# Optimization experiments

Hardware: AMD Instinct MI355X
Metric: run time of the kernel (lower is better)

## Reference

```python
import jax, jax.numpy as jnp
import numpy as np

EMBED = 768; HEADS = 12; MLP = 3072
WL_IN = 4        # activation bits (signed)
WL_W = 4         # weight bits (bit-sliced into 1-bit RRAM cells)
ADC = 5          # ADC precision for each analog partial sum
SUBARRAY = 128   # crossbar subArray rows
ONOFF = 10.0     # conductance on/off ratio
VARI = 0.02      # conductance variability
EPS = 1e-5


def _adc_quant(y, bits):
    # Linear ADC quantization over the full observed range.
    ymax = jnp.max(jnp.abs(y))
    step = ymax / (2 ** bits - 1)
    step = jnp.where(step > 0, step, jnp.ones_like(step))
    return jnp.round(y / step) * step


def _qlinear(x, W, b, key):
    # RRAM crossbar simulated linear layer. x: [T, Fin], W: [Fout, Fin].
    upper, lower = 1.0, 1.0 / ONOFF
    T, Fin = x.shape
    Fout = W.shape[0]
    Wlev = 2 ** WL_W - 1
    Xlev = 2 ** (WL_IN - 1) - 1
    # --- weight -> unsigned integer levels -> binary cell conductances ---
    wmax = jnp.max(jnp.abs(W))
    Wdec = jnp.round((W / wmax + 1.0) * 0.5 * Wlev).astype(jnp.int32)   # [Fout,Fin] in [0,Wlev]
    kb = jnp.arange(WL_W)
    wbits = ((Wdec[:, :, None] >> kb) & 1).astype(x.dtype)              # [Fout,Fin,K]
    noise = VARI * jax.random.normal(key, wbits.shape, dtype=x.dtype)   # conductance variability
    cond = (wbits * (upper - lower) + lower) * (1.0 + noise)
    dummy = 0.5 * (upper + lower)                                       # dummy column conductance
    # --- activation -> signed integer -> magnitude bit slices ---
    xmax = jnp.max(jnp.abs(x))
    Xq = jnp.round(x / xmax * Xlev).astype(jnp.int32)
    sgn = jnp.sign(Xq).astype(x.dtype)
    zb = jnp.arange(WL_IN - 1)
    xbits = ((jnp.abs(Xq)[:, :, None] >> zb) & 1).astype(x.dtype) * sgn[:, :, None]  # [T,Fin,Z]
    # --- subArray partitioning along input dim ---
    pad = (-Fin) % SUBARRAY
    if pad:
        xbits = jnp.pad(xbits, ((0, 0), (0, pad), (0, 0)))
        cond = jnp.pad(cond, ((0, 0), (0, pad), (0, 0)))
    nc = (Fin + pad) // SUBARRAY
    xb = xbits.reshape(T, nc, SUBARRAY, WL_IN - 1)
    cb = cond.reshape(Fout, nc, SUBARRAY, WL_W)
    # analog MAC per subarray, per (input bit z, weight cell k)
    partial = jnp.einsum('tcsz,ocsk->tcozk', xb, cb)                    # [T,nc,Fout,Z,K]
    dummyP = dummy * xb.sum(axis=2)                                     # [T,nc,Z]
    partialQ = _adc_quant(partial, ADC)
    dummyQ = _adc_quant(dummyP, ADC)
    net = partialQ - dummyQ[:, :, None, :, None]                        # recenter to signed weights
    scale = (2.0 ** zb)[:, None] * (2.0 ** kb)[None, :]                 # [Z,K] shift-add
    acc = jnp.einsum('tcozk,zk->to', net, scale)
    out = acc * (xmax / Xlev) * (2.0 * wmax / ((upper - lower) * Wlev))
    return out + b


def _layernorm(x, g, b):
    mu = jnp.mean(x, axis=-1, keepdims=True)
    var = jnp.var(x, axis=-1, keepdims=True)
    return (x - mu) * jax.lax.rsqrt(var + EPS) * g + b


def _attention(x, in_w, in_b, out_w, out_b):
    L, N, E = x.shape
    D = E // HEADS
    qkv = x @ in_w.T + in_b                                             # [L,N,3E]
    q, k, v = jnp.split(qkv, 3, axis=-1)
    q = q.reshape(L, N, HEADS, D)
    k = k.reshape(L, N, HEADS, D)
    v = v.reshape(L, N, HEADS, D)
    scores = jnp.einsum('lnhd,mnhd->nhlm', q, k) / jnp.sqrt(jnp.asarray(D, x.dtype))
    attn = jax.nn.softmax(scores, axis=-1)
    ctx = jnp.einsum('nhlm,mnhd->lnhd', attn, v).reshape(L, N, E)
    return ctx @ out_w.T + out_b


def setup_inputs() -> dict:
    key = jax.random.key(0)
    ks = jax.random.split(key, 8)
    s = 0.02
    return {
        'x': jax.random.normal(ks[0], (256, 2, EMBED), jnp.float32),
        'in_proj_w': s * jax.random.normal(ks[1], (3 * EMBED, EMBED), jnp.float32),
        'in_proj_b': jnp.zeros((3 * EMBED,), jnp.float32),
        'out_proj_w': s * jax.random.normal(ks[2], (EMBED, EMBED), jnp.float32),
        'out_proj_b': jnp.zeros((EMBED,), jnp.float32),
        'ln1_g': jnp.ones((EMBED,), jnp.float32),
        'ln1_b': jnp.zeros((EMBED,), jnp.float32),
        'W1': s * jax.random.normal(ks[3], (MLP, EMBED), jnp.float32),
        'b1': jnp.zeros((MLP,), jnp.float32),
        'W2': s * jax.random.normal(ks[4], (EMBED, MLP), jnp.float32),
        'b2': jnp.zeros((EMBED,), jnp.float32),
        'ln2_g': jnp.ones((EMBED,), jnp.float32),
        'ln2_b': jnp.zeros((EMBED,), jnp.float32),
    }


def reference(x, in_proj_w, in_proj_b, out_proj_w, out_proj_b,
              ln1_g, ln1_b, W1, b1, W2, b2, ln2_g, ln2_b):
    L, N, E = x.shape
    a = _attention(x, in_proj_w, in_proj_b, out_proj_w, out_proj_b)
    h = _layernorm(x + a, ln1_g, ln1_b)
    t = h.reshape(L * N, E)
    m = _qlinear(t, W1, b1, jax.random.key(1))
    m = jax.nn.gelu(m, approximate=False)   # torch nn.GELU default = exact erf
    m = _qlinear(m, W2, b2, jax.random.key(2))
    m = m.reshape(L, N, E)
    return _layernorm(h + m, ln2_g, ln2_b)
```

## Files before the change

### kernel.cpp

```cpp
#include <hip/hip_runtime.h>
#include <math.h>
#include <stdint.h>

#define TOK   512
#define EMB   768
#define QKVD  2304
#define NHEAD 12
#define HD    64
#define MLPD  3072
#define SUBA  128

#define OFF_QKV      0ull
#define OFF_SCORES   9437184ull
#define OFF_CTX      22020096ull
#define OFF_H1PRE    25165824ull
#define OFF_H1       26738688ull
#define OFF_M1       28311552ull
#define OFF_X2       34603008ull
#define OFF_M2       40894464ull
#define OFF_DQ1      42467328ull
#define OFF_DQ2      42504192ull
#define OFF_SCAL     42651648ull
#define OFF_NOISE1   42651712ull
#define OFF_NOISE2   80400448ull
#define OFF_SUMXB1   118149184ull
#define OFF_SUMXB2   118186048ull
#define OFF_WDEC1    118333504ull
#define OFF_WDEC2    120692800ull
#define OFF_XQT1     123052096ull
#define OFF_XQT2     123445312ull
#define WS_NEEDED    125018176ull


__device__ __forceinline__ void blockMaxAtomic(double v, unsigned long long* slot, double* red){
  int tid = threadIdx.x;
  red[tid] = v; __syncthreads();
  for (int st = 128; st > 0; st >>= 1){
    if (tid < st){ double o = red[tid+st]; if (o > red[tid]) red[tid] = o; }
    __syncthreads();
  }
  if (tid == 0) atomicMax(slot, (unsigned long long)__double_as_longlong(red[0]));
}

__device__ __forceinline__ double readSlot(const unsigned long long* s){
  return __longlong_as_double((long long)(*s));
}

__device__ __forceinline__ float xla_exp_f32(float _x){
  float x = fminf(_x, 88.3762626647950f);
  x = fmaxf(x, -88.3762626647949f);
  float m = floorf(fmaf(x, 1.44269504088896341f, 0.5f));
  float r = fmaf(m, -0.6931471805599453f, x);
  float r2 = __fmul_rn(r, r);
  float r3 = __fmul_rn(r2, r);
  float y  = fmaf(1.9875691500e-4f, r, 1.3981999507e-3f);
  float y1 = fmaf(4.1665795894e-2f, r, 1.6666665459e-1f);
  float y2 = __fadd_rn(r, 1.0f);
  y  = fmaf(y, r, 8.3334519073e-3f);
  y1 = fmaf(y1, r, 5.0000001201e-1f);
  y  = fmaf(y, r3, y1);
  y  = fmaf(y, r2, y2);
  int mi = (int)m;
  float two_m = __uint_as_float((unsigned)((mi + 127) << 23));
  float res = __fmul_rn(y, two_m);
  return fmaxf(res, _x);
}

__device__ __forceinline__ float xla_erf_f32(float v){
  float x = fmaxf(fminf(v, 4.0f), -4.0f);
  float x2 = __fmul_rn(x, x);
  float p = fmaf(x2, -2.72614225801306e-10f, 2.77068142495902e-08f);
  p = fmaf(x2, p, -2.10102402082508e-06f);
  p = fmaf(x2, p, -5.69250639462346e-05f);
  p = fmaf(x2, p, -7.34990630326855e-04f);
  p = fmaf(x2, p, -2.95459980854025e-03f);
  p = fmaf(x2, p, -1.60960333262415e-02f);
  p = __fmul_rn(x, p);
  float q = fmaf(x2, -1.45660718464996e-05f, -2.13374055278905e-04f);
  q = fmaf(x2, q, -1.68282697438203e-03f);
  q = fmaf(x2, q, -7.37332916720468e-03f);
  q = fmaf(x2, q, -1.42647390514189e-02f);
  return __fdiv_rn(p, q);
}

__device__ __forceinline__ uint32_t rotl32(uint32_t x, int r){ return (x << r) | (x >> (32 - r)); }

__device__ __forceinline__ void threefry2x32(uint32_t k0, uint32_t k1,
                                             uint32_t x0, uint32_t x1,
                                             uint32_t& o0, uint32_t& o1){
  uint32_t ks2 = k0 ^ k1 ^ 0x1BD11BDAu;
  x0 += k0; x1 += k1;
#define TF_R(r) { x0 += x1; x1 = rotl32(x1, r); x1 ^= x0; }
  TF_R(13) TF_R(15) TF_R(26) TF_R(6)
  x0 += k1; x1 += ks2 + 1u;
  TF_R(17) TF_R(29) TF_R(16) TF_R(24)
  x0 += ks2; x1 += k0 + 2u;
  TF_R(13) TF_R(15) TF_R(26) TF_R(6)
  x0 += k0; x1 += k1 + 3u;
  TF_R(17) TF_R(29) TF_R(16) TF_R(24)
  x0 += k1; x1 += ks2 + 4u;
  TF_R(13) TF_R(15) TF_R(26) TF_R(6)
  x0 += ks2; x1 += k0 + 5u;
#undef TF_R
  o0 = x0; o1 = x1;
}

__device__ float bits_to_noise(uint32_t bits){
  uint32_t fb = (bits >> 9) | 0x3f800000u;
  float f = __uint_as_float(fb);
  f = __fadd_rn(f, -1.0f);
  const float lo = -0.99999994f;
  float u = __fadd_rn(__fmul_rn(f, 2.0f), lo);
  u = fmaxf(lo, u);
  float x  = u;
  float xx = __fmul_rn(x, x);
  float nx = -xx;
  float l1p;
  if (fabsf(nx) < 1e-4f){
    l1p = __fmul_rn(__fadd_rn(__fmul_rn(-0.5f, nx), 1.0f), nx);
  } else {
    float u1 = __fadd_rn(nx, 1.0f);
    l1p = (float)log((double)u1);
  }
  float w = -l1p;
  float p;
  if (w < 5.0f){
    w = __fadd_rn(w, -2.5f);
    p = 2.81022636e-08f;
    p = __fadd_rn(3.43273939e-07f, __fmul_rn(p, w));
    p = __fadd_rn(-3.5233877e-06f,  __fmul_rn(p, w));
    p = __fadd_rn(-4.39150654e-06f, __fmul_rn(p, w));
    p = __fadd_rn(0.00021858087f,   __fmul_rn(p, w));
    p = __fadd_rn(-0.00125372503f,  __fmul_rn(p, w));
    p = __fadd_rn(-0.00417768164f,  __fmul_rn(p, w));
    p = __fadd_rn(0.246640727f,     __fmul_rn(p, w));
    p = __fadd_rn(1.50140941f,      __fmul_rn(p, w));
  } else {
    float sw = __fsqrt_rn(w);
    w = __fadd_rn(sw, -3.0f);
    p = -0.000200214257f;
    p = __fadd_rn(0.000100950558f, __fmul_rn(p, w));
    p = __fadd_rn(0.00134934322f,  __fmul_rn(p, w));
    p = __fadd_rn(-0.00367342844f, __fmul_rn(p, w));
    p = __fadd_rn(0.00573950773f,  __fmul_rn(p, w));
    p = __fadd_rn(-0.0076224613f,  __fmul_rn(p, w));
    p = __fadd_rn(0.00943887047f,  __fmul_rn(p, w));
    p = __fadd_rn(1.00167406f,     __fmul_rn(p, w));
    p = __fadd_rn(2.83297682f,     __fmul_rn(p, w));
  }
  float ei  = __fmul_rn(p, x);
  float nrm = __fmul_rn(1.41421354f, ei);
  return __fmul_rn(0.02f, nrm);
}

__global__ void absmax_f32_k(const float* p, int n, unsigned long long* slot){
  __shared__ double red[256];
  double m = 0.0;
  for (int i = blockIdx.x*256 + threadIdx.x; i < n; i += gridDim.x*256){
    double v = fabs((double)p[i]); if (v > m) m = v;
  }
  blockMaxAtomic(m, slot, red);
}

__global__ void noise_gen_k(uint32_t k0, uint32_t k1, unsigned int n, float* noise){
  unsigned int i = blockIdx.x*256u + threadIdx.x;
  if (i >= n) return;
  uint32_t o0, o1;
  threefry2x32(k0, k1, 0u, i, o0, o1);
  noise[i] = bits_to_noise(o0 ^ o1);
}

__global__ void wdec_gen_k(const float* W, int nW, const unsigned long long* wmax_slot,
                           unsigned char* Wdec){
  int i = blockIdx.x*256 + threadIdx.x;
  if (i >= nW) return;
  float wmax = (float)readSlot(wmax_slot);
  float d = __fdiv_rn(W[i], wmax);
  d = __fadd_rn(d, 1.0f);
  d = __fmul_rn(d, 0.5f);
  d = __fmul_rn(d, 15.0f);
  Wdec[i] = (unsigned char)(int)rintf(d);
}

__global__ __launch_bounds__(256) void qkv_gemm_k(const float* x, const float* w, const float* b, float* qkv){
  __shared__ float xt[8][EMB];
  int j  = blockIdx.x*256 + threadIdx.x;
  int t0 = blockIdx.y*8;
  for (int v = threadIdx.x; v < 8*EMB; v += 256){
    int tt = v / EMB, e = v % EMB;
    xt[tt][e] = x[(size_t)(t0+tt)*EMB + e];
  }
  __syncthreads();
  float acc[8] = {0,0,0,0,0,0,0,0};
  const float* wr = w + (size_t)j*EMB;
  for (int e = 0; e < EMB; ++e){
    float wv = wr[e];
#pragma unroll
    for (int tt = 0; tt < 8; ++tt) acc[tt] = fmaf(xt[tt][e], wv, acc[tt]);
  }
  float bv = b[j];
  for (int tt = 0; tt < 8; ++tt)
    qkv[(size_t)(t0+tt)*QKVD + j] = __fadd_rn(acc[tt], bv);
}

__global__ __launch_bounds__(256) void attn_scores_k(const float* qkv, float* sc){
  __shared__ float kt[32][HD+1];
  int nh = blockIdx.x;
  int n  = nh / NHEAD, h = nh % NHEAD;
  int m0 = blockIdx.y * 32;
  int l  = threadIdx.x;
  for (int v = threadIdx.x; v < 32*HD; v += 256){
    int mm = v / HD, d = v % HD;
    kt[mm][d] = qkv[(size_t)((m0+mm)*2 + n)*QKVD + EMB + h*HD + d];
  }
  __syncthreads();
  float acc[32];
#pragma unroll
  for (int mm = 0; mm < 32; ++mm) acc[mm] = 0.0f;
  const float* qrow = qkv + (size_t)(l*2 + n)*QKVD + h*HD;
  for (int d = 0; d < HD; ++d){
    float qv = qrow[d];
#pragma unroll
    for (int mm = 0; mm < 32; ++mm) acc[mm] = fmaf(qv, kt[mm][d], acc[mm]);
  }
  float* srow = sc + ((size_t)nh*256 + l)*256 + m0;
#pragma unroll
  for (int mm = 0; mm < 32; ++mm) srow[mm] = __fdiv_rn(acc[mm], 8.0f);
}

__global__ void softmax_rows_k(float* sc){
  int row = blockIdx.x*256 + threadIdx.x;
  if (row >= 24*256) return;
  float* p = sc + (size_t)row*256;
  float mx = p[0];
  for (int m = 1; m < 256; ++m) mx = fmaxf(mx, p[m]);
  for (int m = 0; m < 256; ++m) p[m] = xla_exp_f32(__fsub_rn(p[m], mx));
  float s = 0.0f;
  for (int m = 0; m < 256; ++m) s = __fadd_rn(s, p[m]);
  for (int m = 0; m < 256; ++m) p[m] = __fdiv_rn(p[m], s);
}

__global__ void attn_ctx_k(const float* sc, const float* qkv, float* ctx){
  int idx = blockIdx.x*256 + threadIdx.x;
  int t = idx / EMB, i = idx % EMB;
  int l = t / 2, n = t % 2, h = i / HD;
  const float* arow = sc + ((size_t)(n*NHEAD + h)*256 + l)*256;
  float acc = 0.0f;
  for (int m = 0; m < 256; ++m)
    acc = fmaf(arow[m], qkv[(size_t)(m*2 + n)*QKVD + 1536 + i], acc);
  ctx[(size_t)t*EMB + i] = acc;
}

__global__ __launch_bounds__(256) void outproj_res_k(const float* ctx, const float* w, const float* b,
                                                     const float* x, float* h1pre){
  __shared__ float ct[8][EMB];
  int e  = blockIdx.x*256 + threadIdx.x;
  int t0 = blockIdx.y*8;
  for (int v = threadIdx.x; v < 8*EMB; v += 256){
    int tt = v / EMB, i = v % EMB;
    ct[tt][i] = ctx[(size_t)(t0+tt)*EMB + i];
  }
  __syncthreads();
  float acc[8] = {0,0,0,0,0,0,0,0};
  const float* wr = w + (size_t)e*EMB;
  for (int i = 0; i < EMB; ++i){
    float wv = wr[i];
#pragma unroll
    for (int tt = 0; tt < 8; ++tt) acc[tt] = fmaf(ct[tt][i], wv, acc[tt]);
  }
  float bv = b[e];
  for (int tt = 0; tt < 8; ++tt){
    size_t t = t0 + tt;
    float af = __fadd_rn(acc[tt], bv);
    h1pre[t*EMB + e] = __fadd_rn(x[t*EMB + e], af);
  }
}

__global__ void ln_rows_k(const float* in, const float* g, const float* b, float* out){
  int t = blockIdx.x*256 + threadIdx.x;
  if (t >= TOK) return;
  const float* p = in + (size_t)t*EMB;
  float s = 0.0f;
  for (int e = 0; e < EMB; ++e) s = __fadd_rn(s, p[e]);
  float mu = __fdiv_rn(s, 768.0f);
  float s2 = 0.0f;
  for (int e = 0; e < EMB; ++e){
    float d = __fsub_rn(p[e], mu);
    s2 = __fadd_rn(s2, __fmul_rn(d, d));
  }
  float var = __fdiv_rn(s2, 768.0f);
  float rs = __fdiv_rn(1.0f, __fsqrt_rn(__fadd_rn(var, 1e-5f)));
  for (int e = 0; e < EMB; ++e){
    float d = __fsub_rn(p[e], mu);
    out[(size_t)t*EMB + e] = __fadd_rn(__fmul_rn(__fmul_rn(d, rs), g[e]), b[e]);
  }
}

__global__ void final_ln_rows_k(const float* h1, const float* m2T, const float* g, const float* b, float* out){
  int t = blockIdx.x*256 + threadIdx.x;
  if (t >= TOK) return;
  const float* p = h1 + (size_t)t*EMB;
  float s = 0.0f;
  for (int e = 0; e < EMB; ++e) s = __fadd_rn(s, __fadd_rn(p[e], m2T[(size_t)e*TOK + t]));
  float mu = __fdiv_rn(s, 768.0f);
  float s2 = 0.0f;
  for (int e = 0; e < EMB; ++e){
    float d = __fsub_rn(__fadd_rn(p[e], m2T[(size_t)e*TOK + t]), mu);
    s2 = __fadd_rn(s2, __fmul_rn(d, d));
  }
  float var = __fdiv_rn(s2, 768.0f);
  float rs = __fdiv_rn(1.0f, __fsqrt_rn(__fadd_rn(var, 1e-5f)));
  for (int e = 0; e < EMB; ++e){
    float d = __fsub_rn(__fadd_rn(p[e], m2T[(size_t)e*TOK + t]), mu);
    out[(size_t)t*EMB + e] = __fadd_rn(__fmul_rn(__fmul_rn(d, rs), g[e]), b[e]);
  }
}

__global__ void quantx_k(const float* val, const unsigned long long* xmax_slot, int Fin,
                         signed char* XqT){
  int idx = blockIdx.x*256 + threadIdx.x;
  if (idx >= TOK*Fin) return;
  int t = idx / Fin, i = idx % Fin;
  float xmax = (float)readSlot(xmax_slot);
  float u = __fmul_rn(__fdiv_rn(val[idx], xmax), 7.0f);
  XqT[(size_t)i*TOK + t] = (signed char)(int)rintf(u);
}

__global__ void quantxT_k(const float* valT, const unsigned long long* xmax_slot, int n,
                          signed char* XqT){
  int idx = blockIdx.x*256 + threadIdx.x;
  if (idx >= n) return;
  float xmax = (float)readSlot(xmax_slot);
  float u = __fmul_rn(__fdiv_rn(valT[idx], xmax), 7.0f);
  XqT[idx] = (signed char)(int)rintf(u);
}

__global__ void sumxb_k(const signed char* XqT, int NC, int* sumxb, unsigned long long* dmax_slot){
  int idx = blockIdx.x*256 + threadIdx.x;
  if (idx >= TOK*NC) return;
  int t = idx / NC, c = idx % NC;
  int n0 = 0, n1 = 0, n2 = 0;
  for (int s = 0; s < SUBA; ++s){
    int q = XqT[(size_t)(c*SUBA + s)*TOK + t];
    int a = q < 0 ? -q : q;
    int sg = (q > 0) - (q < 0);
    n0 += (a & 1) * sg; n1 += ((a >> 1) & 1) * sg; n2 += ((a >> 2) & 1) * sg;
  }
  sumxb[idx*3 + 0] = n0; sumxb[idx*3 + 1] = n1; sumxb[idx*3 + 2] = n2;
  float d0 = fabsf(__fmul_rn(0.55f, (float)n0));
  float d1 = fabsf(__fmul_rn(0.55f, (float)n1));
  float d2 = fabsf(__fmul_rn(0.55f, (float)n2));
  float m = fmaxf(d0, fmaxf(d1, d2));
  atomicMax(dmax_slot, (unsigned long long)__double_as_longlong((double)m));
}

__global__ void dummyq_k(const int* sumxb, int NC, const unsigned long long* dmax_slot, float* dqT){
  int idx = blockIdx.x*256 + threadIdx.x;
  if (idx >= TOK*NC*3) return;
  int t = idx / (NC*3);
  int r = idx % (NC*3);
  int c = r / 3, z = r % 3;
  float dmax = (float)readSlot(dmax_slot);
  float step = __fdiv_rn(dmax, 31.0f);
  if (!(step > 0.0f)) step = 1.0f;
  float P = __fmul_rn(0.55f, (float)sumxb[idx]);
  dqT[((size_t)c*3 + z)*TOK + t] = __fmul_rn(rintf(__fdiv_rn(P, step)), step);
}

template<int OTILE>
__device__ __forceinline__ void qlin_stage(const signed char* XqT, const unsigned char* Wdec,
                                           const float* noise, int Fin, int c, int o0, int t0,
                                           signed char* xq, float (*cond)[SUBA][4]){
  const int tid = threadIdx.x;
  const uint32_t* src = (const uint32_t*)(XqT + (size_t)c*SUBA*TOK + t0);
  uint32_t* dst = (uint32_t*)xq;
  for (int j = tid; j < SUBA*64; j += 256){
    int s = j >> 6, dw = j & 63;
    dst[s*64 + dw] = src[s*128 + dw];
  }
  for (int v = tid; v < OTILE*SUBA*4; v += 256){
    int o = v >> 9;
    int r = v & 511;
    int s = r >> 2, k = r & 3;
    size_t i = (size_t)(o0+o)*Fin + c*SUBA + s;
    float bit = (float)((Wdec[i] >> k) & 1);
    float nz  = noise[i*4 + k];
    cond[o][s][k] = __fmul_rn(__fadd_rn(__fmul_rn(bit, 0.9f), 0.1f), __fadd_rn(1.0f, nz));
  }
}

template<int OTILE>
__device__ __forceinline__ void qlin_acc_c(const signed char* xq, const float (*cond)[SUBA][4],
                                           float (*acc)[12]){
  const int tid = threadIdx.x;
#pragma unroll
  for (int o = 0; o < OTILE; ++o)
#pragma unroll
    for (int r = 0; r < 12; ++r) acc[o][r] = 0.0f;
  for (int s = 0; s < SUBA; ++s){
    int q = xq[s*256 + tid];
    int a = q < 0 ? -q : q;
    int i0 = a & 1, i1 = (a >> 1) & 1, i2 = (a >> 2) & 1;
    if (q < 0){ i0 = -i0; i1 = -i1; i2 = -i2; }
    float b0 = (float)i0, b1 = (float)i1, b2 = (float)i2;
#pragma unroll
    for (int o = 0; o < OTILE; ++o){
      const float4 cv = *(const float4*)&cond[o][s][0];
      acc[o][0]  = fmaf(b0, cv.x, acc[o][0]);
      acc[o][1]  = fmaf(b0, cv.y, acc[o][1]);
      acc[o][2]  = fmaf(b0, cv.z, acc[o][2]);
      acc[o][3]  = fmaf(b0, cv.w, acc[o][3]);
      acc[o][4]  = fmaf(b1, cv.x, acc[o][4]);
      acc[o][5]  = fmaf(b1, cv.y, acc[o][5]);
      acc[o][6]  = fmaf(b1, cv.z, acc[o][6]);
      acc[o][7]  = fmaf(b1, cv.w, acc[o][7]);
      acc[o][8]  = fmaf(b2, cv.x, acc[o][8]);
      acc[o][9]  = fmaf(b2, cv.y, acc[o][9]);
      acc[o][10] = fmaf(b2, cv.z, acc[o][10]);
      acc[o][11] = fmaf(b2, cv.w, acc[o][11]);
    }
  }
}

template<int OTILE>
__global__ __launch_bounds__(256) void qlin_pass1_t(const signed char* XqT, const unsigned char* Wdec,
                                                    const float* noise, int Fin, int NC,
                                                    unsigned long long* ymax_slot){
  __shared__ signed char xq[SUBA*256];
  __shared__ float cond[OTILE][SUBA][4];
  __shared__ double red[256];
  const int o0 = blockIdx.x*OTILE;
  const int t0 = blockIdx.y*256;
  float acc[OTILE][12];
  float lmax = 0.0f;
  for (int c = 0; c < NC; ++c){
    __syncthreads();
    qlin_stage<OTILE>(XqT, Wdec, noise, Fin, c, o0, t0, xq, cond);
    __syncthreads();
    qlin_acc_c<OTILE>(xq, cond, acc);
#pragma unroll
    for (int o = 0; o < OTILE; ++o)
#pragma unroll
      for (int r = 0; r < 12; ++r) lmax = fmaxf(lmax, fabsf(acc[o][r]));
  }
  blockMaxAtomic((double)lmax, ymax_slot, red);
}

template<int OTILE>
__global__ __launch_bounds__(256) void qlin_pass2_t(const signed char* XqT, const unsigned char* Wdec,
                                                    const float* noise, const float* dqT, const float* bias,
                                                    int Fin, int NC,
                                                    const unsigned long long* ymax_slot,
                                                    const unsigned long long* xmax_slot,
                                                    const unsigned long long* wmax_slot,
                                                    float* outT){
  __shared__ signed char xq[SUBA*256];
  __shared__ float cond[OTILE][SUBA][4];
  const int o0 = blockIdx.x*OTILE;
  const int t0 = blockIdx.y*256;
  const int t  = t0 + threadIdx.x;
  float ymax = (float)readSlot(ymax_slot);
  float step = __fdiv_rn(ymax, 31.0f);
  if (!(step > 0.0f)) step = 1.0f;
  float acc[OTILE][12];
  float netsum[OTILE][12];
#pragma unroll
  for (int o = 0; o < OTILE; ++o)
#pragma unroll
    for (int r = 0; r < 12; ++r) netsum[o][r] = 0.0f;
  for (int c = 0; c < NC; ++c){
    __syncthreads();
    qlin_stage<OTILE>(XqT, Wdec, noise, Fin, c, o0, t0, xq, cond);
    __syncthreads();
    qlin_acc_c<OTILE>(xq, cond, acc);
    float dqv[3];
#pragma unroll
    for (int z = 0; z < 3; ++z) dqv[z] = dqT[((size_t)c*3 + z)*TOK + t];
#pragma unroll
    for (int o = 0; o < OTILE; ++o)
#pragma unroll
      for (int z = 0; z < 3; ++z)
#pragma unroll
        for (int k = 0; k < 4; ++k){
          float pq  = __fmul_rn(rintf(__fdiv_rn(acc[o][z*4+k], step)), step);
          float net = __fsub_rn(pq, dqv[z]);
          netsum[o][z*4+k] = __fadd_rn(netsum[o][z*4+k], net);
        }
  }
  float xmax = (float)readSlot(xmax_slot);
  float wmax = (float)readSlot(wmax_slot);
  float A = __fdiv_rn(xmax, 7.0f);
  float B = __fdiv_rn(__fmul_rn(2.0f, wmax), 13.5f);
#pragma unroll
  for (int o = 0; o < OTILE; ++o){
    float tot = 0.0f;
#pragma unroll
    for (int z = 0; z < 3; ++z)
#pragma unroll
      for (int k = 0; k < 4; ++k)
        tot = __fadd_rn(tot, __fmul_rn(netsum[o][z*4+k], (float)(1 << (z + k))));
    float outv = __fadd_rn(__fmul_rn(__fmul_rn(tot, A), B), bias[o0+o]);
    outT[(size_t)(o0+o)*TOK + t] = outv;
  }
}

__global__ void gelu_absmax_k(const float* m1, int n, float* x2, unsigned long long* xmax_slot){
  __shared__ double red[256];
  double m = 0.0;
  for (int i = blockIdx.x*256 + threadIdx.x; i < n; i += gridDim.x*256){
    float v = m1[i];
    float t1 = __fdiv_rn(v, 1.4142135623730951f);
    float e = xla_erf_f32(t1);
    float s = __fadd_rn(e, 1.0f);
    float g = __fdiv_rn(__fmul_rn(v, s), 2.0f);
    x2[i] = g;
    double a = fabs((double)g); if (a > m) m = a;
  }
  blockMaxAtomic(m, xmax_slot, red);
}

extern "C" void kernel_launch(void* const* d_in, const int* in_sizes, int n_in,
                              void* d_out, int out_size, void* d_ws, size_t ws_size,
                              hipStream_t stream){
  if (ws_size < WS_NEEDED) return;
  const float* x      = (const float*)d_in[0];
  const float* in_w   = (const float*)d_in[1];
  const float* in_b   = (const float*)d_in[2];
  const float* out_w  = (const float*)d_in[3];
  const float* out_b  = (const float*)d_in[4];
  const float* ln1_g  = (const float*)d_in[5];
  const float* ln1_b  = (const float*)d_in[6];
  const float* W1     = (const float*)d_in[7];
  const float* b1     = (const float*)d_in[8];
  const float* W2     = (const float*)d_in[9];
  const float* b2     = (const float*)d_in[10];
  const float* ln2_g  = (const float*)d_in[11];
  const float* ln2_b  = (const float*)d_in[12];

  char* ws = (char*)d_ws;
  float* qkv    = (float*)(ws + OFF_QKV);
  float* scores = (float*)(ws + OFF_SCORES);
  float* ctx    = (float*)(ws + OFF_CTX);
  float* h1pre  = (float*)(ws + OFF_H1PRE);
  float* h1     = (float*)(ws + OFF_H1);
  float* m1     = (float*)(ws + OFF_M1);
  float* x2     = (float*)(ws + OFF_X2);
  float* m2     = (float*)(ws + OFF_M2);
  float* dq1    = (float*)(ws + OFF_DQ1);
  float* dq2    = (float*)(ws + OFF_DQ2);
  unsigned long long* scal = (unsigned long long*)(ws + OFF_SCAL);
  float* noise1  = (float*)(ws + OFF_NOISE1);
  float* noise2  = (float*)(ws + OFF_NOISE2);
  int*   sumxb1  = (int*)(ws + OFF_SUMXB1);
  int*   sumxb2  = (int*)(ws + OFF_SUMXB2);
  unsigned char* wdec1 = (unsigned char*)(ws + OFF_WDEC1);
  unsigned char* wdec2 = (unsigned char*)(ws + OFF_WDEC2);
  signed char* xqt1 = (signed char*)(ws + OFF_XQT1);
  signed char* xqt2 = (signed char*)(ws + OFF_XQT2);

  hipMemsetAsync(scal, 0, 64, stream);

  absmax_f32_k<<<1024,256,0,stream>>>(W1, MLPD*EMB, scal+0);
  absmax_f32_k<<<1024,256,0,stream>>>(W2, EMB*MLPD, scal+1);

  noise_gen_k<<<36864,256,0,stream>>>(0u, 1u, 9437184u, noise1);
  noise_gen_k<<<36864,256,0,stream>>>(0u, 2u, 9437184u, noise2);
  wdec_gen_k<<<9216,256,0,stream>>>(W1, MLPD*EMB, scal+0, wdec1);
  wdec_gen_k<<<9216,256,0,stream>>>(W2, EMB*MLPD, scal+1, wdec2);

  qkv_gemm_k<<<dim3(9,64),256,0,stream>>>(x, in_w, in_b, qkv);
  attn_scores_k<<<dim3(24,8),256,0,stream>>>(qkv, scores);
  softmax_rows_k<<<24,256,0,stream>>>(scores);
  attn_ctx_k<<<1536,256,0,stream>>>(scores, qkv, ctx);
  outproj_res_k<<<dim3(3,64),256,0,stream>>>(ctx, out_w, out_b, x, h1pre);
  ln_rows_k<<<2,256,0,stream>>>(h1pre, ln1_g, ln1_b, h1);

  absmax_f32_k<<<1024,256,0,stream>>>(h1, TOK*EMB, scal+2);
  quantx_k<<<(TOK*EMB+255)/256,256,0,stream>>>(h1, scal+2, EMB, xqt1);
  sumxb_k<<<(TOK*6+255)/256,256,0,stream>>>(xqt1, 6, sumxb1, scal+4);
  dummyq_k<<<(TOK*6*3+255)/256,256,0,stream>>>(sumxb1, 6, scal+4, dq1);
  qlin_pass1_t<8><<<dim3(MLPD/8,2),256,0,stream>>>(xqt1, wdec1, noise1, EMB, 6, scal+3);
  qlin_pass2_t<4><<<dim3(MLPD/4,2),256,0,stream>>>(xqt1, wdec1, noise1, dq1, b1,
                                                   EMB, 6, scal+3, scal+2, scal+0, m1);

  gelu_absmax_k<<<6144,256,0,stream>>>(m1, TOK*MLPD, x2, scal+5);
  quantxT_k<<<(TOK*MLPD+255)/256,256,0,stream>>>(x2, scal+5, TOK*MLPD, xqt2);
  sumxb_k<<<(TOK*24+255)/256,256,0,stream>>>(xqt2, 24, sumxb2, scal+7);
  dummyq_k<<<(TOK*24*3+255)/256,256,0,stream>>>(sumxb2, 24, scal+7, dq2);
  qlin_pass1_t<4><<<dim3(EMB/4,2),256,0,stream>>>(xqt2, wdec2, noise2, MLPD, 24, scal+6);
  qlin_pass2_t<4><<<dim3(EMB/4,2),256,0,stream>>>(xqt2, wdec2, noise2, dq2, b2,
                                                  MLPD, 24, scal+6, scal+5, scal+1, m2);

  final_ln_rows_k<<<2,256,0,stream>>>(h1, m2, ln2_g, ln2_b, (float*)d_out);
}
```

Measured before the change: 3.157 ms.

## Use packed FP32 FMA, tile GEMM weights in LDS, split pass1 over chunks

Replaces the scalar FMAs in the dense GEMMs, attention scores, attention context and the crossbar accumulation with two-wide packed FMA vectors (v_pk_fma_f32 on CDNA). The QKV and out-projection GEMMs are merged into one kernel that stages 32-wide K tiles of the weights in padded LDS rather than reading weight rows straight from global memory. The K tile in attention scores is transposed so that vector loads from it are contiguous, and attn_ctx now computes two outputs per thread. The ADC max pass1 kernels gain a z grid dimension that splits subarray chunks across blocks, which adds parallelism at the cost of more atomicMax operations.

```diff
diff --git a/kernel.cpp b/kernel.cpp
--- a/kernel.cpp
+++ b/kernel.cpp
@@ -31,6 +31,16 @@
 #define OFF_XQT2     123445312ull
 #define WS_NEEDED    125018176ull
 
+
+typedef float f32x2 __attribute__((ext_vector_type(2)));
+
+__device__ __forceinline__ f32x2 pkfma(f32x2 a, f32x2 b, f32x2 c){
+#if __has_builtin(__builtin_elementwise_fma)
+  return __builtin_elementwise_fma(a, b, c);
+#else
+  f32x2 r; r.x = fmaf(a.x, b.x, c.x); r.y = fmaf(a.y, b.y, c.y); return r;
+#endif
+}
 
 __device__ __forceinline__ void blockMaxAtomic(double v, unsigned long long* slot, double* red){
   int tid = threadIdx.x;
@@ -182,50 +192,79 @@
   Wdec[i] = (unsigned char)(int)rintf(d);
 }
 
-__global__ __launch_bounds__(256) void qkv_gemm_k(const float* x, const float* w, const float* b, float* qkv){
-  __shared__ float xt[8][EMB];
-  int j  = blockIdx.x*256 + threadIdx.x;
-  int t0 = blockIdx.y*8;
-  for (int v = threadIdx.x; v < 8*EMB; v += 256){
-    int tt = v / EMB, e = v % EMB;
-    xt[tt][e] = x[(size_t)(t0+tt)*EMB + e];
-  }
-  __syncthreads();
-  float acc[8] = {0,0,0,0,0,0,0,0};
-  const float* wr = w + (size_t)j*EMB;
-  for (int e = 0; e < EMB; ++e){
-    float wv = wr[e];
-#pragma unroll
-    for (int tt = 0; tt < 8; ++tt) acc[tt] = fmaf(xt[tt][e], wv, acc[tt]);
-  }
-  float bv = b[j];
-  for (int tt = 0; tt < 8; ++tt)
-    qkv[(size_t)(t0+tt)*QKVD + j] = __fadd_rn(acc[tt], bv);
+#define KTILE 32
+__global__ __launch_bounds__(256) void gemm8_k(const float* src, const float* w, const float* bias,
+                                               const float* resid, float* out, int N, int K){
+  __shared__ float xt[EMB*8];
+  __shared__ float wl[256*(KTILE+1)];
+  const int tid = threadIdx.x;
+  const int j  = blockIdx.x*256 + tid;
+  const int t0 = blockIdx.y*8;
+  for (int v = tid; v < K*8; v += 256){
+    int e = v >> 3, tt = v & 7;
+    xt[v] = src[(size_t)(t0+tt)*K + e];
+  }
+  f32x2 acc[4] = {{0.f,0.f},{0.f,0.f},{0.f,0.f},{0.f,0.f}};
+  const int ntile = K / KTILE;
+  for (int et = 0; et < ntile; ++et){
+    __syncthreads();
+    for (int v = tid; v < 256*KTILE; v += 256){
+      int r = v >> 5, cc = v & 31;
+      wl[r*(KTILE+1) + cc] = w[(size_t)(blockIdx.x*256 + r)*K + et*KTILE + cc];
+    }
+    __syncthreads();
+    for (int ee = 0; ee < KTILE; ++ee){
+      float wv = wl[tid*(KTILE+1) + ee];
+      f32x2 wv2 = {wv, wv};
+      const f32x2* xp = (const f32x2*)&xt[(et*KTILE + ee)*8];
+#pragma unroll
+      for (int q = 0; q < 4; ++q) acc[q] = pkfma(xp[q], wv2, acc[q]);
+    }
+  }
+  float bv = bias[j];
+#pragma unroll
+  for (int q = 0; q < 4; ++q){
+    float a0 = __fadd_rn(acc[q].x, bv);
+    float a1 = __fadd_rn(acc[q].y, bv);
+    size_t ta = (size_t)(t0 + q*2), tb = ta + 1;
+    if (resid){
+      out[ta*N + j] = __fadd_rn(resid[ta*N + j], a0);
+      out[tb*N + j] = __fadd_rn(resid[tb*N + j], a1);
+    } else {
+      out[ta*N + j] = a0;
+      out[tb*N + j] = a1;
+    }
+  }
 }
 
 __global__ __launch_bounds__(256) void attn_scores_k(const float* qkv, float* sc){
-  __shared__ float kt[32][HD+1];
+  __shared__ float kt[64][34];
   int nh = blockIdx.x;
   int n  = nh / NHEAD, h = nh % NHEAD;
   int m0 = blockIdx.y * 32;
   int l  = threadIdx.x;
-  for (int v = threadIdx.x; v < 32*HD; v += 256){
-    int mm = v / HD, d = v % HD;
-    kt[mm][d] = qkv[(size_t)((m0+mm)*2 + n)*QKVD + EMB + h*HD + d];
+  for (int v = threadIdx.x; v < 32*64; v += 256){
+    int mm = v >> 6, d = v & 63;
+    kt[d][mm] = qkv[(size_t)((m0+mm)*2 + n)*QKVD + EMB + h*HD + d];
   }
   __syncthreads();
-  float acc[32];
-#pragma unroll
-  for (int mm = 0; mm < 32; ++mm) acc[mm] = 0.0f;
+  f32x2 acc[16];
+#pragma unroll
+  for (int i = 0; i < 16; ++i) acc[i] = {0.f,0.f};
   const float* qrow = qkv + (size_t)(l*2 + n)*QKVD + h*HD;
   for (int d = 0; d < HD; ++d){
     float qv = qrow[d];
-#pragma unroll
-    for (int mm = 0; mm < 32; ++mm) acc[mm] = fmaf(qv, kt[mm][d], acc[mm]);
+    f32x2 q2 = {qv, qv};
+    const f32x2* kp = (const f32x2*)&kt[d][0];
+#pragma unroll
+    for (int i = 0; i < 16; ++i) acc[i] = pkfma(q2, kp[i], acc[i]);
   }
   float* srow = sc + ((size_t)nh*256 + l)*256 + m0;
 #pragma unroll
-  for (int mm = 0; mm < 32; ++mm) srow[mm] = __fdiv_rn(acc[mm], 8.0f);
+  for (int i = 0; i < 16; ++i){
+    srow[2*i]   = __fdiv_rn(acc[i].x, 8.0f);
+    srow[2*i+1] = __fdiv_rn(acc[i].y, 8.0f);
+  }
 }
 
 __global__ void softmax_rows_k(float* sc){
@@ -242,38 +281,19 @@
 
 __global__ void attn_ctx_k(const float* sc, const float* qkv, float* ctx){
   int idx = blockIdx.x*256 + threadIdx.x;
-  int t = idx / EMB, i = idx % EMB;
-  int l = t / 2, n = t % 2, h = i / HD;
+  int t = idx / 384, i2 = idx % 384;
+  int i = i2*2;
+  int l = t >> 1, n = t & 1, h = i >> 6;
   const float* arow = sc + ((size_t)(n*NHEAD + h)*256 + l)*256;
-  float acc = 0.0f;
-  for (int m = 0; m < 256; ++m)
-    acc = fmaf(arow[m], qkv[(size_t)(m*2 + n)*QKVD + 1536 + i], acc);
-  ctx[(size_t)t*EMB + i] = acc;
-}
-
-__global__ __launch_bounds__(256) void outproj_res_k(const float* ctx, const float* w, const float* b,
-                                                     const float* x, float* h1pre){
-  __shared__ float ct[8][EMB];
-  int e  = blockIdx.x*256 + threadIdx.x;
-  int t0 = blockIdx.y*8;
-  for (int v = threadIdx.x; v < 8*EMB; v += 256){
-    int tt = v / EMB, i = v % EMB;
-    ct[tt][i] = ctx[(size_t)(t0+tt)*EMB + i];
-  }
-  __syncthreads();
-  float acc[8] = {0,0,0,0,0,0,0,0};
-  const float* wr = w + (size_t)e*EMB;
-  for (int i = 0; i < EMB; ++i){
-    float wv = wr[i];
-#pragma unroll
-    for (int tt = 0; tt < 8; ++tt) acc[tt] = fmaf(ct[tt][i], wv, acc[tt]);
-  }
-  float bv = b[e];
-  for (int tt = 0; tt < 8; ++tt){
-    size_t t = t0 + tt;
-    float af = __fadd_rn(acc[tt], bv);
-    h1pre[t*EMB + e] = __fadd_rn(x[t*EMB + e], af);
-  }
+  f32x2 acc = {0.f,0.f};
+  for (int m = 0; m < 256; ++m){
+    float av = arow[m];
+    f32x2 a2 = {av, av};
+    f32x2 v2 = *(const f32x2*)&qkv[(size_t)(m*2 + n)*QKVD + 1536 + i];
+    acc = pkfma(a2, v2, acc);
+  }
+  ctx[(size_t)t*EMB + i]     = acc.x;
+  ctx[(size_t)t*EMB + i + 1] = acc.y;
 }
 
 __global__ void ln_rows_k(const float* in, const float* g, const float* b, float* out){
@@ -391,49 +411,46 @@
 
 template<int OTILE>
 __device__ __forceinline__ void qlin_acc_c(const signed char* xq, const float (*cond)[SUBA][4],
-                                           float (*acc)[12]){
+                                           f32x2 (*acc)[6]){
   const int tid = threadIdx.x;
 #pragma unroll
   for (int o = 0; o < OTILE; ++o)
 #pragma unroll
-    for (int r = 0; r < 12; ++r) acc[o][r] = 0.0f;
+    for (int r = 0; r < 6; ++r) acc[o][r] = {0.f,0.f};
   for (int s = 0; s < SUBA; ++s){
     int q = xq[s*256 + tid];
     int a = q < 0 ? -q : q;
     int i0 = a & 1, i1 = (a >> 1) & 1, i2 = (a >> 2) & 1;
     if (q < 0){ i0 = -i0; i1 = -i1; i2 = -i2; }
-    float b0 = (float)i0, b1 = (float)i1, b2 = (float)i2;
+    float f0 = (float)i0, f1 = (float)i1, f2 = (float)i2;
+    f32x2 b0 = {f0, f0}, b1 = {f1, f1}, b2 = {f2, f2};
 #pragma unroll
     for (int o = 0; o < OTILE; ++o){
-      const float4 cv = *(const float4*)&cond[o][s][0];
-      acc[o][0]  = fmaf(b0, cv.x, acc[o][0]);
-      acc[o][1]  = fmaf(b0, cv.y, acc[o][1]);
-      acc[o][2]  = fmaf(b0, cv.z, acc[o][2]);
-      acc[o][3]  = fmaf(b0, cv.w, acc[o][3]);
-      acc[o][4]  = fmaf(b1, cv.x, acc[o][4]);
-      acc[o][5]  = fmaf(b1, cv.y, acc[o][5]);
-      acc[o][6]  = fmaf(b1, cv.z, acc[o][6]);
-      acc[o][7]  = fmaf(b1, cv.w, acc[o][7]);
-      acc[o][8]  = fmaf(b2, cv.x, acc[o][8]);
-      acc[o][9]  = fmaf(b2, cv.y, acc[o][9]);
-      acc[o][10] = fmaf(b2, cv.z, acc[o][10]);
-      acc[o][11] = fmaf(b2, cv.w, acc[o][11]);
+      const f32x2* cp = (const f32x2*)&cond[o][s][0];
+      f32x2 c01 = cp[0], c23 = cp[1];
+      acc[o][0] = pkfma(b0, c01, acc[o][0]);
+      acc[o][1] = pkfma(b0, c23, acc[o][1]);
+      acc[o][2] = pkfma(b1, c01, acc[o][2]);
+      acc[o][3] = pkfma(b1, c23, acc[o][3]);
+      acc[o][4] = pkfma(b2, c01, acc[o][4]);
+      acc[o][5] = pkfma(b2, c23, acc[o][5]);
     }
   }
 }
 
-template<int OTILE>
+template<int OTILE, int CCHUNK>
 __global__ __launch_bounds__(256) void qlin_pass1_t(const signed char* XqT, const unsigned char* Wdec,
-                                                    const float* noise, int Fin, int NC,
+                                                    const float* noise, int Fin,
                                                     unsigned long long* ymax_slot){
   __shared__ signed char xq[SUBA*256];
   __shared__ float cond[OTILE][SUBA][4];
   __shared__ double red[256];
   const int o0 = blockIdx.x*OTILE;
   const int t0 = blockIdx.y*256;
-  float acc[OTILE][12];
+  const int c0 = blockIdx.z*CCHUNK;
+  f32x2 acc[OTILE][6];
   float lmax = 0.0f;
-  for (int c = 0; c < NC; ++c){
+  for (int c = c0; c < c0 + CCHUNK; ++c){
     __syncthreads();
     qlin_stage<OTILE>(XqT, Wdec, noise, Fin, c, o0, t0, xq, cond);
     __syncthreads();
@@ -441,7 +458,10 @@
 #pragma unroll
     for (int o = 0; o < OTILE; ++o)
 #pragma unroll
-      for (int r = 0; r < 12; ++r) lmax = fmaxf(lmax, fabsf(acc[o][r]));
+      for (int r = 0; r < 6; ++r){
+        lmax = fmaxf(lmax, fabsf(acc[o][r].x));
+        lmax = fmaxf(lmax, fabsf(acc[o][r].y));
+      }
   }
   blockMaxAtomic((double)lmax, ymax_slot, red);
 }
@@ -462,7 +482,7 @@
   float ymax = (float)readSlot(ymax_slot);
   float step = __fdiv_rn(ymax, 31.0f);
   if (!(step > 0.0f)) step = 1.0f;
-  float acc[OTILE][12];
+  f32x2 acc[OTILE][6];
   float netsum[OTILE][12];
 #pragma unroll
   for (int o = 0; o < OTILE; ++o)
@@ -482,7 +502,9 @@
       for (int z = 0; z < 3; ++z)
 #pragma unroll
         for (int k = 0; k < 4; ++k){
-          float pq  = __fmul_rn(rintf(__fdiv_rn(acc[o][z*4+k], step)), step);
+          f32x2 av2 = acc[o][z*2 + (k >> 1)];
+          float av = (k & 1) ? av2.y : av2.x;
+          float pq  = __fmul_rn(rintf(__fdiv_rn(av, step)), step);
           float net = __fsub_rn(pq, dqv[z]);
           netsum[o][z*4+k] = __fadd_rn(netsum[o][z*4+k], net);
         }
@@ -568,18 +590,18 @@
   wdec_gen_k<<<9216,256,0,stream>>>(W1, MLPD*EMB, scal+0, wdec1);
   wdec_gen_k<<<9216,256,0,stream>>>(W2, EMB*MLPD, scal+1, wdec2);
 
-  qkv_gemm_k<<<dim3(9,64),256,0,stream>>>(x, in_w, in_b, qkv);
+  gemm8_k<<<dim3(9,64),256,0,stream>>>(x, in_w, in_b, nullptr, qkv, QKVD, EMB);
   attn_scores_k<<<dim3(24,8),256,0,stream>>>(qkv, scores);
   softmax_rows_k<<<24,256,0,stream>>>(scores);
-  attn_ctx_k<<<1536,256,0,stream>>>(scores, qkv, ctx);
-  outproj_res_k<<<dim3(3,64),256,0,stream>>>(ctx, out_w, out_b, x, h1pre);
+  attn_ctx_k<<<768,256,0,stream>>>(scores, qkv, ctx);
+  gemm8_k<<<dim3(3,64),256,0,stream>>>(ctx, out_w, out_b, x, h1pre, EMB, EMB);
   ln_rows_k<<<2,256,0,stream>>>(h1pre, ln1_g, ln1_b, h1);
 
   absmax_f32_k<<<1024,256,0,stream>>>(h1, TOK*EMB, scal+2);
   quantx_k<<<(TOK*EMB+255)/256,256,0,stream>>>(h1, scal+2, EMB, xqt1);
   sumxb_k<<<(TOK*6+255)/256,256,0,stream>>>(xqt1, 6, sumxb1, scal+4);
   dummyq_k<<<(TOK*6*3+255)/256,256,0,stream>>>(sumxb1, 6, scal+4, dq1);
-  qlin_pass1_t<8><<<dim3(MLPD/8,2),256,0,stream>>>(xqt1, wdec1, noise1, EMB, 6, scal+3);
+  qlin_pass1_t<8,3><<<dim3(MLPD/8,2,2),256,0,stream>>>(xqt1, wdec1, noise1, EMB, scal+3);
   qlin_pass2_t<4><<<dim3(MLPD/4,2),256,0,stream>>>(xqt1, wdec1, noise1, dq1, b1,
                                                    EMB, 6, scal+3, scal+2, scal+0, m1);
 
@@ -587,7 +609,7 @@
   quantxT_k<<<(TOK*MLPD+255)/256,256,0,stream>>>(x2, scal+5, TOK*MLPD, xqt2);
   sumxb_k<<<(TOK*24+255)/256,256,0,stream>>>(xqt2, 24, sumxb2, scal+7);
   dummyq_k<<<(TOK*24*3+255)/256,256,0,stream>>>(sumxb2, 24, scal+7, dq2);
-  qlin_pass1_t<4><<<dim3(EMB/4,2),256,0,stream>>>(xqt2, wdec2, noise2, MLPD, 24, scal+6);
+  qlin_pass1_t<4,6><<<dim3(EMB/4,2,4),256,0,stream>>>(xqt2, wdec2, noise2, MLPD, scal+6);
   qlin_pass2_t<4><<<dim3(EMB/4,2),256,0,stream>>>(xqt2, wdec2, noise2, dq2, b2,
                                                   MLPD, 24, scal+6, scal+5, scal+1, m2);
 
```

Result: no change. 3.149 ms (-0.2%).
